# Optimization experiments

Hardware: AMD Instinct MI355X
Metric: run time of the kernel (lower is better)

Reference implementation:

```python
import jax, jax.numpy as jnp
import numpy as np
from math import sqrt

B, S, D, H = 4, 2048, 1024, 16
DH = D // H          # 64
DF = 4 * D           # 4096
EPS = 1e-5
NEG = -1e9


def layer_norm(x, w, b):
    mu = jnp.mean(x, axis=-1, keepdims=True)
    var = jnp.mean((x - mu) ** 2, axis=-1, keepdims=True)
    return (x - mu) * jax.lax.rsqrt(var + EPS) * w + b


def setup_inputs() -> dict:
    key = jax.random.key(0)
    ks = jax.random.split(key, 16)
    s = 0.02
    return {
        "state": jax.random.normal(ks[0], (B, S, D), jnp.float32),
        "mask": jax.random.randint(ks[1], (B, S), 0, 2, jnp.int32),
        "ln1_w": jnp.ones((D,), jnp.float32),
        "ln1_b": jnp.zeros((D,), jnp.float32),
        "Wq": jax.random.normal(ks[2], (H, D, DH), jnp.float32) * s,
        "bq": jnp.zeros((H, DH), jnp.float32),
        "Wk": jax.random.normal(ks[3], (H, D, DH), jnp.float32) * s,
        "bk": jnp.zeros((H, DH), jnp.float32),
        "Wv": jax.random.normal(ks[4], (H, D, DH), jnp.float32) * s,
        "bv": jnp.zeros((H, DH), jnp.float32),
        "Wo": jax.random.normal(ks[5], (D, D), jnp.float32) * s,
        "bo": jnp.zeros((D,), jnp.float32),
        "ln2_w": jnp.ones((D,), jnp.float32),
        "ln2_b": jnp.zeros((D,), jnp.float32),
        "W1": jax.random.normal(ks[6], (D, DF), jnp.float32) * s,
        "b1": jnp.zeros((DF,), jnp.float32),
        "W2": jax.random.normal(ks[7], (DF, D), jnp.float32) * s,
        "b2": jnp.zeros((D,), jnp.float32),
    }


def reference(state, mask, ln1_w, ln1_b, Wq, bq, Wk, bk, Wv, bv, Wo, bo,
              ln2_w, ln2_b, W1, b1, W2, b2):
    # pre-norm attention block
    hidden = layer_norm(state, ln1_w, ln1_b)               # [B,S,D]
    q = jnp.einsum("bsd,hde->bhse", hidden, Wq) + bq[None, :, None, :]
    k = jnp.einsum("bsd,hde->bhse", hidden, Wk) + bk[None, :, None, :]
    v = jnp.einsum("bsd,hde->bhse", hidden, Wv) + bv[None, :, None, :]
    scores = jnp.einsum("bhse,bhte->bhst", q, k) / sqrt(DH)  # [B,H,S,S]
    scores = jnp.where(mask[:, None, None, :] == 0, NEG, scores)
    weights = jax.nn.softmax(scores, axis=-1)
    attended = jnp.einsum("bhst,bhte->bhse", weights, v)    # [B,H,S,DH]
    # concat heads in head order (matches torch cat over per-head outputs)
    attended = attended.transpose(0, 2, 1, 3).reshape(B, S, D)
    attn_out = attended @ Wo + bo
    output = state + attn_out
    # pre-norm FFN block (dropout=0 -> identity)
    hidden = layer_norm(output, ln2_w, ln2_b)
    ff = jax.nn.gelu(hidden @ W1 + b1, approximate=False) @ W2 + b2
    return output + ff
```

## Files before the change

kernel.cpp:

```cpp
#include <hip/hip_runtime.h>
#include <math.h>

#define B_  4
#define S_  2048
#define D_  1024
#define H_  16
#define DH_ 64
#define DF_ 4096
#define M_  8192

#define QSC 0.18033688011112042f

typedef __attribute__((ext_vector_type(8))) short bf8_t;
typedef __attribute__((ext_vector_type(4))) float f4_t;

#if defined(__has_builtin)
#if __has_builtin(__builtin_amdgcn_cvt_pk_bf16_f32)
#define HAVE_PKCVT 1
#endif
#if __has_builtin(__builtin_amdgcn_global_load_lds)
#define HAVE_ASYNC 1
#endif
#if __has_builtin(__builtin_amdgcn_exp2f)
#define EXP2F(x) __builtin_amdgcn_exp2f(x)
#else
#define EXP2F(x) __expf((x) * 0.69314718055994531f)
#endif
#else
#define EXP2F(x) __expf((x) * 0.69314718055994531f)
#endif

__device__ __forceinline__ unsigned pk_bf16(float lo, float hi) {
#ifdef HAVE_PKCVT
  auto r = __builtin_amdgcn_cvt_pk_bf16_f32(lo, hi);
  unsigned u; __builtin_memcpy(&u, &r, 4); return u;
#else
  union { float f; unsigned u; } a, b2; a.f = lo; b2.f = hi;
  unsigned ra = a.u + 0x7fffu + ((a.u >> 16) & 1u);
  unsigned rb = b2.u + 0x7fffu + ((b2.u >> 16) & 1u);
  return (ra >> 16) | (rb & 0xffff0000u);
#endif
}

__device__ __forceinline__ unsigned short f2bf(float x) {
  return (unsigned short)(pk_bf16(x, x) & 0xffffu);
}

__device__ __forceinline__ bf8_t upk8(unsigned u0, unsigned u1, unsigned u2, unsigned u3) {
  union { unsigned u[4]; bf8_t v; } c;
  c.u[0] = u0; c.u[1] = u1; c.u[2] = u2; c.u[3] = u3; return c.v;
}

__device__ __forceinline__ f4_t mfma32(bf8_t a, bf8_t b, f4_t c) {
  return __builtin_amdgcn_mfma_f32_16x16x32_bf16(a, b, c, 0, 0, 0);
}

__device__ __forceinline__ void async16(const void* g, void* l) {
#ifdef HAVE_ASYNC
  __builtin_amdgcn_global_load_lds((__attribute__((address_space(1))) void*)(g),
                                   (__attribute__((address_space(3))) void*)(l), 16, 0, 0);
#else
  *(uint4*)l = *(const uint4*)g;
#endif
}

__device__ __forceinline__ int sw(int row) { return row & 7; }


__global__ __launch_bounds__(256) void wtrans_kernel(const float* __restrict__ in,
                                                     unsigned short* __restrict__ out,
                                                     int K, int N) {
  const int k0 = blockIdx.x * 32, n0 = blockIdx.y * 32;
  __shared__ float t[32][33];
  const int tid = threadIdx.x;
#pragma unroll
  for (int i = 0; i < 4; i++) {
    int idx = i * 256 + tid; int r = idx >> 5, c = idx & 31;
    t[r][c] = in[(size_t)(k0 + r) * N + n0 + c];
  }
  __syncthreads();
#pragma unroll
  for (int i = 0; i < 4; i++) {
    int idx = i * 256 + tid; int r = idx >> 5, c = idx & 31;
    out[(size_t)(n0 + r) * K + k0 + c] = f2bf(t[c][r]);
  }
}

__global__ __launch_bounds__(256) void qkvpack_kernel(const float* __restrict__ Wq,
                                                      const float* __restrict__ Wk,
                                                      const float* __restrict__ Wv,
                                                      unsigned short* __restrict__ WqkvT) {
  const int z = blockIdx.z;
  const int sel = z >> 4, h = z & 15;
  const float* in = (sel == 0 ? Wq : sel == 1 ? Wk : Wv) + (size_t)h * D_ * DH_;
  const int k0 = blockIdx.x * 32, n0 = blockIdx.y * 32;
  __shared__ float t[32][33];
  const int tid = threadIdx.x;
#pragma unroll
  for (int i = 0; i < 4; i++) {
    int idx = i * 256 + tid; int r = idx >> 5, c = idx & 31;
    t[r][c] = in[(size_t)(k0 + r) * DH_ + n0 + c];
  }
  __syncthreads();
#pragma unroll
  for (int i = 0; i < 4; i++) {
    int idx = i * 256 + tid; int r = idx >> 5, c = idx & 31;
    int n = sel * 1024 + h * 64 + n0 + r;
    WqkvT[(size_t)n * D_ + k0 + c] = f2bf(t[c][r]);
  }
}

__global__ void biaspack_kernel(const float* __restrict__ bq, const float* __restrict__ bk,
                                const float* __restrict__ bv, float* __restrict__ bqkv) {
  int i = blockIdx.x * 256 + threadIdx.x;
  if (i < 3072) {
    int sel = i >> 10, j = i & 1023;
    const float* src = sel == 0 ? bq : sel == 1 ? bk : bv;
    bqkv[i] = src[j];
  }
}


__global__ __launch_bounds__(256) void ln_kernel(const float* __restrict__ x,
                                                 const float* __restrict__ w,
                                                 const float* __restrict__ bb,
                                                 unsigned short* __restrict__ out) {
  const int row = blockIdx.x;
  const float* xr = x + (size_t)row * D_;
  const int tid = threadIdx.x;
  float v[4]; float s = 0.f;
#pragma unroll
  for (int i = 0; i < 4; i++) { v[i] = xr[tid + i * 256]; s += v[i]; }
  __shared__ float red[8];
#pragma unroll
  for (int o = 32; o; o >>= 1) s += __shfl_xor(s, o, 64);
  const int wv = tid >> 6, ln = tid & 63;
  if (!ln) red[wv] = s;
  __syncthreads();
  float mean = (red[0] + red[1] + red[2] + red[3]) * (1.f / 1024.f);
  float s2 = 0.f;
#pragma unroll
  for (int i = 0; i < 4; i++) { float d = v[i] - mean; s2 += d * d; }
#pragma unroll
  for (int o = 32; o; o >>= 1) s2 += __shfl_xor(s2, o, 64);
  if (!ln) red[4 + wv] = s2;
  __syncthreads();
  float var = (red[4] + red[5] + red[6] + red[7]) * (1.f / 1024.f);
  float rstd = rsqrtf(var + 1e-5f);
#pragma unroll
  for (int i = 0; i < 4; i++) {
    int c = tid + i * 256;
    out[(size_t)row * D_ + c] = f2bf((v[i] - mean) * rstd * w[c] + bb[c]);
  }
}

template <int EPI>
__global__ __launch_bounds__(256) void gemm_bt(const unsigned short* __restrict__ A,
                                               const unsigned short* __restrict__ Bt,
                                               const float* __restrict__ bias,
                                               const float* __restrict__ resid,
                                               unsigned short* __restrict__ outb,
                                               float* __restrict__ outf,
                                               unsigned short* __restrict__ vTout,
                                               int Ndim, int Kdim) {
  __shared__ __align__(16) unsigned short Asmem[4096];
  __shared__ __align__(16) unsigned short Bsmem[4096];
  const int tid = threadIdx.x;
  const int wave = tid >> 6, lane = tid & 63;
  const int quad = lane >> 4, l16 = lane & 15;
  const int wm = wave >> 1, wn = wave & 1;
  const int m0 = blockIdx.y * 128, n0 = blockIdx.x * 128;

  const f4_t fzero = {0.f, 0.f, 0.f, 0.f};
  f4_t acc[4][4];
#pragma unroll
  for (int i = 0; i < 4; i++)
#pragma unroll
    for (int j = 0; j < 4; j++) acc[i][j] = fzero;

  const int rowA = tid >> 2;
  const int kp = (tid & 3) * 8;

  for (int k0 = 0; k0 < Kdim; k0 += 32) {
    __syncthreads();
#pragma unroll
    for (int r = 0; r < 2; r++) {
      const int row = r * 64 + rowA;
      const int e = row * 32 + kp;
      async16(A  + (size_t)(m0 + row) * Kdim + k0 + kp, &Asmem[e]);
      async16(Bt + (size_t)(n0 + row) * Kdim + k0 + kp, &Bsmem[e]);
    }
    __syncthreads();

    bf8_t a[4], b[4];
#pragma unroll
    for (int i = 0; i < 4; i++) {
      a[i] = *(const bf8_t*)&Asmem[(wm * 64 + i * 16 + l16) * 32 + quad * 8];
      b[i] = *(const bf8_t*)&Bsmem[(wn * 64 + i * 16 + l16) * 32 + quad * 8];
    }
#pragma unroll
    for (int i = 0; i < 4; i++)
#pragma unroll
      for (int j = 0; j < 4; j++)
        acc[i][j] = mfma32(a[i], b[j], acc[i][j]);
  }

  const float sc = 1.f;
#pragma unroll
  for (int i = 0; i < 4; i++) {
#pragma unroll
    for (int j = 0; j < 4; j++) {
#pragma unroll
      for (int r = 0; r < 4; r++) {
        const int m = m0 + wm * 64 + i * 16 + quad * 4 + r;
        const int n = n0 + wn * 64 + j * 16 + l16;
        float v = acc[i][j][r] + bias[n];
        (void)sc;
        if constexpr (EPI == 2) v = 0.5f * v * (1.f + erff(v * 0.70710678118654752f));
        if constexpr (EPI == 1) {
          v += resid[(size_t)m * Ndim + n];
          outf[(size_t)m * Ndim + n] = v;
        } else {
          outb[(size_t)m * Ndim + n] = f2bf(v);
        }
      }
    }
  }
  (void)vTout;
}

template <int EPI>
__global__ __launch_bounds__(512, 2) void gemm256(const unsigned short* __restrict__ A,
                                                  const unsigned short* __restrict__ Bt,
                                                  const float* __restrict__ bias,
                                                  const float* __restrict__ resid,
                                                  unsigned short* __restrict__ outb,
                                                  float* __restrict__ outf,
                                                  unsigned short* __restrict__ vTout,
                                                  int Ndim, int Kdim) {
  __shared__ __align__(16) unsigned short Asm[32768];
  __shared__ __align__(16) unsigned short Bsm[32768];
  const int tid = threadIdx.x;
  const int wave = tid >> 6, lane = tid & 63;
  const int quad = lane >> 4, l16 = lane & 15;
  const int wm = wave >> 2, wn = wave & 3;

  const int gx = gridDim.x;
  const int nwg = gx * (int)gridDim.y;
  const int lin = (int)blockIdx.y * gx + (int)blockIdx.x;
  const int swz = (lin & 7) * (nwg >> 3) + (lin >> 3);
  const int m0 = (swz / gx) * 256, n0 = (swz % gx) * 256;

  const int NT = Kdim >> 6;
  const int srow = lane >> 3, schk = lane & 7;

#define STAGE_A(t, row0) do {                                                   \
    const int r_ = (row0) + srow;                                               \
    async16(A + (size_t)(m0 + r_) * Kdim + (t) * 64 + ((schk ^ (r_ & 7)) << 3), \
            &Asm[(((t) & 1) << 14) + ((row0) << 6)]); } while (0)
#define STAGE_B(t, row0) do {                                                    \
    const int r_ = (row0) + srow;                                                \
    async16(Bt + (size_t)(n0 + r_) * Kdim + (t) * 64 + ((schk ^ (r_ & 7)) << 3), \
            &Bsm[(((t) & 1) << 14) + ((row0) << 6)]); } while (0)
#define STAGE_A0(t) do { STAGE_A(t, wave * 8); STAGE_A(t, 128 + wave * 8); } while (0)
#define STAGE_A1(t) do { STAGE_A(t, 64 + wave * 8); STAGE_A(t, 192 + wave * 8); } while (0)
#define STAGE_B0(t) do { const int rb_ = (wave >> 1) * 64 + (wave & 1) * 8;  \
    STAGE_B(t, rb_); STAGE_B(t, rb_ + 16); } while (0)
#define STAGE_B1(t) do { const int rb_ = (wave >> 1) * 64 + 32 + (wave & 1) * 8; \
    STAGE_B(t, rb_); STAGE_B(t, rb_ + 16); } while (0)

#define AFR(bo, row, s) \
  (*(const bf8_t*)&Asm[(bo) + ((row) << 6) + ((((s) * 4 + quad) ^ ((row) & 7)) << 3)])
#define BFR(bo, row, s) \
  (*(const bf8_t*)&Bsm[(bo) + ((row) << 6) + ((((s) * 4 + quad) ^ ((row) & 7)) << 3)])

  const f4_t fzero = {0.f, 0.f, 0.f, 0.f};
  f4_t acc[8][4];
#pragma unroll
  for (int i = 0; i < 8; i++)
#pragma unroll
    for (int j = 0; j < 4; j++) acc[i][j] = fzero;

  STAGE_A0(0); STAGE_A1(0); STAGE_B0(0); STAGE_B1(0);
  STAGE_A0(1); STAGE_A1(1); STAGE_B0(1); STAGE_B1(1);
  asm volatile("s_waitcnt vmcnt(8)" ::: "memory");
  __builtin_amdgcn_s_barrier();

  const int ar0 = wm << 7;
  const int br0 = wn << 6;

  for (int t = 0; t < NT; ++t) {
    const int bo = (t & 1) << 14;
    const bool pf = (t + 2) < NT;
    const int t2 = t + 2;
    bf8_t af[4][2], bf0[2][2], bf1[2][2];

#pragma unroll
    for (int i = 0; i < 4; i++) {
      af[i][0] = AFR(bo, ar0 + i * 16 + l16, 0);
      af[i][1] = AFR(bo, ar0 + i * 16 + l16, 1);
    }
#pragma unroll
    for (int j = 0; j < 2; j++) {
      bf0[j][0] = BFR(bo, br0 + j * 16 + l16, 0);
      bf0[j][1] = BFR(bo, br0 + j * 16 + l16, 1);
    }
    asm volatile("s_waitcnt lgkmcnt(8)" ::: "memory");
    __builtin_amdgcn_s_barrier();
    asm volatile("s_waitcnt lgkmcnt(0)" ::: "memory");
    __builtin_amdgcn_sched_barrier(0);
    __builtin_amdgcn_s_setprio(1);
#pragma unroll
    for (int s = 0; s < 2; s++)
#pragma unroll
      for (int i = 0; i < 4; i++)
#pragma unroll
        for (int j = 0; j < 2; j++)
          acc[i][j] = mfma32(af[i][s], bf0[j][s], acc[i][j]);
    __builtin_amdgcn_s_setprio(0);
    __builtin_amdgcn_s_barrier();

#pragma unroll
    for (int j = 0; j < 2; j++) {
      bf1[j][0] = BFR(bo, br0 + 32 + j * 16 + l16, 0);
      bf1[j][1] = BFR(bo, br0 + 32 + j * 16 + l16, 1);
    }
    if (pf) { STAGE_A0(t2); STAGE_B0(t2); }
    __builtin_amdgcn_s_barrier();
    asm volatile("s_waitcnt lgkmcnt(0)" ::: "memory");
    __builtin_amdgcn_sched_barrier(0);
    __builtin_amdgcn_s_setprio(1);
#pragma unroll
    for (int s = 0; s < 2; s++)
#pragma unroll
      for (int i = 0; i < 4; i++)
#pragma unroll
        for (int j = 0; j < 2; j++)
          acc[i][2 + j] = mfma32(af[i][s], bf1[j][s], acc[i][2 + j]);
    __builtin_amdgcn_s_setprio(0);
    __builtin_amdgcn_s_barrier();

#pragma unroll
    for (int i = 0; i < 4; i++) {
      af[i][0] = AFR(bo, ar0 + 64 + i * 16 + l16, 0);
      af[i][1] = AFR(bo, ar0 + 64 + i * 16 + l16, 1);
    }
    if (pf) STAGE_B1(t2);
    __builtin_amdgcn_s_barrier();
    asm volatile("s_waitcnt lgkmcnt(0)" ::: "memory");
    __builtin_amdgcn_sched_barrier(0);
    __builtin_amdgcn_s_setprio(1);
#pragma unroll
    for (int s = 0; s < 2; s++)
#pragma unroll
      for (int i = 0; i < 4; i++)
#pragma unroll
        for (int j = 0; j < 2; j++)
          acc[4 + i][2 + j] = mfma32(af[i][s], bf1[j][s], acc[4 + i][2 + j]);
    __builtin_amdgcn_s_setprio(0);
    __builtin_amdgcn_s_barrier();

    if (pf) STAGE_A1(t2);
    __builtin_amdgcn_s_barrier();
    __builtin_amdgcn_s_setprio(1);
#pragma unroll
    for (int s = 0; s < 2; s++)
#pragma unroll
      for (int i = 0; i < 4; i++)
#pragma unroll
        for (int j = 0; j < 2; j++)
          acc[4 + i][j] = mfma32(af[i][s], bf0[j][s], acc[4 + i][j]);
    __builtin_amdgcn_s_setprio(0);
    if (pf) asm volatile("s_waitcnt vmcnt(8)" ::: "memory");
    else    asm volatile("s_waitcnt vmcnt(0)" ::: "memory");
    __builtin_amdgcn_s_barrier();
  }

#undef STAGE_A
#undef STAGE_B
#undef STAGE_A0
#undef STAGE_A1
#undef STAGE_B0
#undef STAGE_B1
#undef AFR
#undef BFR

  if (EPI == 0 && n0 >= 2048) {
    const int bb2 = m0 >> 11;
    const int sb64 = (m0 & 2047) + (wm << 7);
#pragma unroll
    for (int mi = 0; mi < 8; mi++) {
      const int i4 = mi & 3;
      const int g0 = (i4 & 2) * 16 + 8 * quad + 4 * (i4 & 1);
      const int sbase = sb64 + (mi >> 2) * 64 + g0;
#pragma unroll
      for (int nj = 0; nj < 4; nj++) {
        const int n = n0 + wn * 64 + nj * 16 + l16;
        const int ef = n - 2048;
        const int hh = ef >> 6, e = ef & 63;
        const float bsv = bias[n];
        uint2 wq;
        wq.x = pk_bf16(acc[mi][nj][0] + bsv, acc[mi][nj][1] + bsv);
        wq.y = pk_bf16(acc[mi][nj][2] + bsv, acc[mi][nj][3] + bsv);
        *(uint2*)&vTout[(size_t)((bb2 * 16 + hh) * 64 + e) * S_ + sbase] = wq;
      }
    }
    return;
  }

  const float sc = (EPI == 0 && n0 < 1024) ? QSC : 1.f;
#pragma unroll
  for (int mi = 0; mi < 8; mi++) {
#pragma unroll
    for (int nj = 0; nj < 4; nj++) {
#pragma unroll
      for (int r = 0; r < 4; r++) {
        const int m = m0 + wm * 128 + mi * 16 + quad * 4 + r;
        const int n = n0 + wn * 64 + nj * 16 + l16;
        float v = acc[mi][nj][r] + bias[n];
        if constexpr (EPI == 0) v *= sc;
        if constexpr (EPI == 2) v = 0.5f * v * (1.f + erff(v * 0.70710678118654752f));
        if constexpr (EPI == 1) {
          v += resid[(size_t)m * Ndim + n];
          outf[(size_t)m * Ndim + n] = v;
        } else {
          outb[(size_t)m * Ndim + n] = f2bf(v);
        }
      }
    }
  }
}


__global__ __launch_bounds__(256) void attn_kernel(const unsigned short* __restrict__ qkv,
                                                   const unsigned short* __restrict__ vT,
                                                   const int* __restrict__ maskp,
                                                   unsigned short* __restrict__ attended) {
  const int bh = blockIdx.y, b = bh >> 4, h = bh & 15;
  const int q0 = blockIdx.x * 128;
  const int tid = threadIdx.x, wv = tid >> 6, lane = tid & 63;
  const int quad = lane >> 4, l16 = lane & 15;
  __shared__ __align__(16) unsigned short smem[16384];
  __shared__ float biasl[128];
  unsigned short* Ks = smem;
  unsigned short* Vs = smem + 8192;

  bf8_t aq[2][2];
#pragma unroll
  for (int sb = 0; sb < 2; sb++) {
    const unsigned short* qrow =
        qkv + (size_t)(b * S_ + q0 + wv * 32 + sb * 16 + l16) * 3072 + h * 64;
    aq[sb][0] = *(const bf8_t*)(qrow + quad * 8);
    aq[sb][1] = *(const bf8_t*)(qrow + 32 + quad * 8);
  }

  const bf8_t ones8 = {0x3F80, 0x3F80, 0x3F80, 0x3F80, 0x3F80, 0x3F80, 0x3F80, 0x3F80};
  const f4_t fzero = {0.f, 0.f, 0.f, 0.f};
  f4_t o[2][4], lacc[2];
#pragma unroll
  for (int sb = 0; sb < 2; sb++) {
    lacc[sb] = fzero;
#pragma unroll
    for (int ee = 0; ee < 4; ee++) o[sb][ee] = fzero;
  }

  for (int t0 = 0; t0 < S_; t0 += 128) {
    __syncthreads();
#pragma unroll
    for (int r = 0; r < 4; r++) {
      int ci = r * 256 + tid;
      int krow = ci >> 3, kc = (ci & 7) ^ sw(krow);
      async16(qkv + (size_t)(b * S_ + t0 + krow) * 3072 + 1024 + h * 64 + kc * 8,
              &Ks[ci * 8]);
      int e = ci >> 4, half = (ci >> 3) & 1, vc = (ci & 7) ^ sw(e);
      async16(vT + (size_t)(bh * 64 + e) * S_ + t0 + half * 64 + vc * 8,
              &Vs[ci * 8]);
    }
    if (tid < 128) biasl[tid] = maskp[b * S_ + t0 + tid] ? 0.f : -8e9f;
    __syncthreads();

#pragma unroll
    for (int th = 0; th < 2; th++) {
      f4_t sf[2][4];
#pragma unroll
      for (int jj = 0; jj < 4; jj++) {
        f4_t bi = *(const f4_t*)&biasl[th * 64 + jj * 16 + quad * 4];
        sf[0][jj] = bi;
        sf[1][jj] = bi;
      }
#pragma unroll
      for (int jj = 0; jj < 4; jj++) {
        int krow = th * 64 + jj * 16 + l16, sk = sw(krow);
        bf8_t kf0 = *(const bf8_t*)&Ks[krow * 64 + (quad ^ sk) * 8];
        bf8_t kf1 = *(const bf8_t*)&Ks[krow * 64 + ((quad + 4) ^ sk) * 8];
        sf[0][jj] = mfma32(kf0, aq[0][0], sf[0][jj]);
        sf[0][jj] = mfma32(kf1, aq[0][1], sf[0][jj]);
        sf[1][jj] = mfma32(kf0, aq[1][0], sf[1][jj]);
        sf[1][jj] = mfma32(kf1, aq[1][1], sf[1][jj]);
      }

      bf8_t pp[2][2];
#pragma unroll
      for (int sb = 0; sb < 2; sb++) {
#pragma unroll
        for (int h2 = 0; h2 < 2; h2++) {
          float p0 = EXP2F(sf[sb][2 * h2][0]),     p1 = EXP2F(sf[sb][2 * h2][1]);
          float p2 = EXP2F(sf[sb][2 * h2][2]),     p3 = EXP2F(sf[sb][2 * h2][3]);
          float p4 = EXP2F(sf[sb][2 * h2 + 1][0]), p5 = EXP2F(sf[sb][2 * h2 + 1][1]);
          float p6 = EXP2F(sf[sb][2 * h2 + 1][2]), p7 = EXP2F(sf[sb][2 * h2 + 1][3]);
          pp[sb][h2] = upk8(pk_bf16(p0, p1), pk_bf16(p2, p3),
                            pk_bf16(p4, p5), pk_bf16(p6, p7));
        }
        lacc[sb] = mfma32(ones8, pp[sb][0], lacc[sb]);
        lacc[sb] = mfma32(ones8, pp[sb][1], lacc[sb]);
      }

#pragma unroll
      for (int ee = 0; ee < 4; ee++) {
        int vrow = ee * 16 + l16, sv = sw(vrow);
#pragma unroll
        for (int h2 = 0; h2 < 2; h2++) {
          bf8_t vf = *(const bf8_t*)&Vs[vrow * 128 + th * 64 + ((4 * h2 + quad) ^ sv) * 8];
          o[0][ee] = mfma32(vf, pp[0][h2], o[0][ee]);
          o[1][ee] = mfma32(vf, pp[1][h2], o[1][ee]);
        }
      }
    }
  }

  float linv[2];
#pragma unroll
  for (int sb = 0; sb < 2; sb++) linv[sb] = 1.f / lacc[sb][0];

  __syncthreads();
  unsigned short* Os = smem;
#pragma unroll
  for (int sb = 0; sb < 2; sb++) {
    int srow = wv * 32 + sb * 16 + l16;
#pragma unroll
    for (int ee = 0; ee < 4; ee++) {
      unsigned w0 = pk_bf16(o[sb][ee][0] * linv[sb], o[sb][ee][1] * linv[sb]);
      unsigned w1 = pk_bf16(o[sb][ee][2] * linv[sb], o[sb][ee][3] * linv[sb]);
      uint2 wq; wq.x = w0; wq.y = w1;
      *(uint2*)&Os[srow * 72 + ee * 16 + quad * 4] = wq;
    }
  }
  __syncthreads();
#pragma unroll
  for (int it = 0; it < 4; it++) {
    int row = it * 32 + (tid >> 3), e0 = (tid & 7) * 8;
    bf8_t v = *(const bf8_t*)&Os[row * 72 + e0];
    *(bf8_t*)&attended[(size_t)(b * S_ + q0 + row) * D_ + h * 64 + e0] = v;
  }
}


extern "C" void kernel_launch(void* const* d_in, const int* in_sizes, int n_in,
                              void* d_out, int out_size, void* d_ws, size_t ws_size,
                              hipStream_t stream) {
  const float* state = (const float*)d_in[0];
  const int*   maskp = (const int*)d_in[1];
  const float* ln1w  = (const float*)d_in[2];
  const float* ln1b  = (const float*)d_in[3];
  const float* Wq    = (const float*)d_in[4];
  const float* bq    = (const float*)d_in[5];
  const float* Wk    = (const float*)d_in[6];
  const float* bk    = (const float*)d_in[7];
  const float* Wv    = (const float*)d_in[8];
  const float* bv    = (const float*)d_in[9];
  const float* Wo    = (const float*)d_in[10];
  const float* bo    = (const float*)d_in[11];
  const float* ln2w  = (const float*)d_in[12];
  const float* ln2b  = (const float*)d_in[13];
  const float* W1    = (const float*)d_in[14];
  const float* b1    = (const float*)d_in[15];
  const float* W2    = (const float*)d_in[16];
  const float* b2    = (const float*)d_in[17];

  char* w = (char*)d_ws;
  unsigned short* hidden = (unsigned short*)w; w += (size_t)M_ * D_ * 2;
  unsigned short* qkv    = (unsigned short*)w; w += (size_t)M_ * 3072 * 2;
  unsigned short* vT     = (unsigned short*)w; w += (size_t)M_ * D_ * 2;
  float*          outp   = (float*)w;          w += (size_t)M_ * D_ * 4;
  unsigned short* WqkvT  = (unsigned short*)w; w += (size_t)3072 * D_ * 2;
  unsigned short* WoT    = (unsigned short*)w; w += (size_t)D_ * D_ * 2;
  unsigned short* W1T    = (unsigned short*)w; w += (size_t)DF_ * D_ * 2;
  unsigned short* W2T    = (unsigned short*)w; w += (size_t)D_ * DF_ * 2;
  float*          bqkv   = (float*)w;          w += 3072 * 4;
  unsigned short* ff1    = qkv;

  qkvpack_kernel<<<dim3(32, 2, 48), 256, 0, stream>>>(Wq, Wk, Wv, WqkvT);
  wtrans_kernel<<<dim3(32, 32), 256, 0, stream>>>(Wo, WoT, D_, D_);
  wtrans_kernel<<<dim3(32, 128), 256, 0, stream>>>(W1, W1T, D_, DF_);
  wtrans_kernel<<<dim3(128, 32), 256, 0, stream>>>(W2, W2T, DF_, D_);
  biaspack_kernel<<<12, 256, 0, stream>>>(bq, bk, bv, bqkv);

  ln_kernel<<<M_, 256, 0, stream>>>(state, ln1w, ln1b, hidden);
  gemm256<0><<<dim3(3072 / 256, M_ / 256), 512, 0, stream>>>(hidden, WqkvT, bqkv, nullptr,
                                                             qkv, nullptr, vT, 3072, D_);
  attn_kernel<<<dim3(S_ / 128, B_ * H_), 256, 0, stream>>>(qkv, vT, maskp, hidden);
  gemm_bt<1><<<dim3(D_ / 128, M_ / 128), 256, 0, stream>>>(hidden, WoT, bo, state,
                                                           nullptr, outp, nullptr, D_, D_);
  ln_kernel<<<M_, 256, 0, stream>>>(outp, ln2w, ln2b, hidden);
  gemm256<2><<<dim3(DF_ / 256, M_ / 256), 512, 0, stream>>>(hidden, W1T, b1, nullptr,
                                                            ff1, nullptr, nullptr, DF_, D_);
  gemm_bt<1><<<dim3(D_ / 128, M_ / 128), 256, 0, stream>>>(ff1, W2T, b2, outp,
                                                           nullptr, (float*)d_out, nullptr, D_, DF_);
}
```

Measured before the change: 597.4 us.

## Split-K the FFN down-projection on the 256-tile GEMM and add reduction kernel

The second FFN GEMM (K=4096, N=1024) now runs on the larger 256x256 tile kernel with split-K of 2 along a new grid z dimension. Each half writes fp32 partials into separate buffers, and a small elementwise kernel adds the partials, residual and bias. The aim is to keep enough workgroups in flight for an N=1024 output while using the more efficient tile kernel. It also adds grouped block swizzling to the 128-tile GEMM used by the output projection. In exchange it pays extra fp32 traffic for the partials and one more kernel launch, and it reorders workspace buffers so the partial buffer can reuse the hidden region.

```diff
diff --git a/kernel.cpp b/kernel.cpp
--- a/kernel.cpp
+++ b/kernel.cpp
@@ -154,6 +154,18 @@
   }
 }
 
+__global__ __launch_bounds__(256) void ffn2red_kernel(float* __restrict__ out,
+                                                      const float* __restrict__ P,
+                                                      const float* __restrict__ resid,
+                                                      const float* __restrict__ bias) {
+  const size_t i = ((size_t)blockIdx.x * 256 + threadIdx.x) * 4;
+  f4_t a  = *(const f4_t*)&out[i];
+  f4_t p  = *(const f4_t*)&P[i];
+  f4_t rr = *(const f4_t*)&resid[i];
+  f4_t bb = *(const f4_t*)&bias[(int)(i & 1023)];
+  *(f4_t*)&out[i] = a + p + rr + bb;
+}
+
 template <int EPI>
 __global__ __launch_bounds__(256) void gemm_bt(const unsigned short* __restrict__ A,
                                                const unsigned short* __restrict__ Bt,
@@ -161,7 +173,6 @@
                                                const float* __restrict__ resid,
                                                unsigned short* __restrict__ outb,
                                                float* __restrict__ outf,
-                                               unsigned short* __restrict__ vTout,
                                                int Ndim, int Kdim) {
   __shared__ __align__(16) unsigned short Asmem[4096];
   __shared__ __align__(16) unsigned short Bsmem[4096];
@@ -169,7 +180,12 @@
   const int wave = tid >> 6, lane = tid & 63;
   const int quad = lane >> 4, l16 = lane & 15;
   const int wm = wave >> 1, wn = wave & 1;
-  const int m0 = blockIdx.y * 128, n0 = blockIdx.x * 128;
+
+  const int gx = gridDim.x;
+  const int nwg = gx * (int)gridDim.y;
+  const int lin = (int)blockIdx.y * gx + (int)blockIdx.x;
+  const int swz = (lin & 7) * (nwg >> 3) + (lin >> 3);
+  const int m0 = (swz / gx) * 128, n0 = (swz % gx) * 128;
 
   const f4_t fzero = {0.f, 0.f, 0.f, 0.f};
   f4_t acc[4][4];
@@ -205,7 +221,6 @@
         acc[i][j] = mfma32(a[i], b[j], acc[i][j]);
   }
 
-  const float sc = 1.f;
 #pragma unroll
   for (int i = 0; i < 4; i++) {
 #pragma unroll
@@ -215,7 +230,6 @@
         const int m = m0 + wm * 64 + i * 16 + quad * 4 + r;
         const int n = n0 + wn * 64 + j * 16 + l16;
         float v = acc[i][j][r] + bias[n];
-        (void)sc;
         if constexpr (EPI == 2) v = 0.5f * v * (1.f + erff(v * 0.70710678118654752f));
         if constexpr (EPI == 1) {
           v += resid[(size_t)m * Ndim + n];
@@ -226,7 +240,6 @@
       }
     }
   }
-  (void)vTout;
 }
 
 template <int EPI>
@@ -236,8 +249,9 @@
                                                   const float* __restrict__ resid,
                                                   unsigned short* __restrict__ outb,
                                                   float* __restrict__ outf,
+                                                  float* __restrict__ outf2,
                                                   unsigned short* __restrict__ vTout,
-                                                  int Ndim, int Kdim) {
+                                                  int Ndim, int Kdim, int Kstride) {
   __shared__ __align__(16) unsigned short Asm[32768];
   __shared__ __align__(16) unsigned short Bsm[32768];
   const int tid = threadIdx.x;
@@ -250,17 +264,20 @@
   const int lin = (int)blockIdx.y * gx + (int)blockIdx.x;
   const int swz = (lin & 7) * (nwg >> 3) + (lin >> 3);
   const int m0 = (swz / gx) * 256, n0 = (swz % gx) * 256;
+  const int kz = (int)blockIdx.z * Kdim;
 
   const int NT = Kdim >> 6;
   const int srow = lane >> 3, schk = lane & 7;
 
-#define STAGE_A(t, row0) do {                                                   \
-    const int r_ = (row0) + srow;                                               \
-    async16(A + (size_t)(m0 + r_) * Kdim + (t) * 64 + ((schk ^ (r_ & 7)) << 3), \
+#define STAGE_A(t, row0) do {                                               \
+    const int r_ = (row0) + srow;                                           \
+    async16(A + (size_t)(m0 + r_) * Kstride + kz + (t) * 64 +               \
+                ((schk ^ (r_ & 7)) << 3),                                   \
             &Asm[(((t) & 1) << 14) + ((row0) << 6)]); } while (0)
-#define STAGE_B(t, row0) do {                                                    \
-    const int r_ = (row0) + srow;                                                \
-    async16(Bt + (size_t)(n0 + r_) * Kdim + (t) * 64 + ((schk ^ (r_ & 7)) << 3), \
+#define STAGE_B(t, row0) do {                                               \
+    const int r_ = (row0) + srow;                                           \
+    async16(Bt + (size_t)(n0 + r_) * Kstride + kz + (t) * 64 +              \
+                 ((schk ^ (r_ & 7)) << 3),                                  \
             &Bsm[(((t) & 1) << 14) + ((row0) << 6)]); } while (0)
 #define STAGE_A0(t) do { STAGE_A(t, wave * 8); STAGE_A(t, 128 + wave * 8); } while (0)
 #define STAGE_A1(t) do { STAGE_A(t, 64 + wave * 8); STAGE_A(t, 192 + wave * 8); } while (0)
@@ -408,21 +425,25 @@
     return;
   }
 
+  float* const pdst = (EPI == 3) ? (blockIdx.z ? outf2 : outf) : outf;
   const float sc = (EPI == 0 && n0 < 1024) ? QSC : 1.f;
 #pragma unroll
   for (int mi = 0; mi < 8; mi++) {
 #pragma unroll
     for (int nj = 0; nj < 4; nj++) {
+      const int n = n0 + wn * 64 + nj * 16 + l16;
+      const float bs = (EPI == 3) ? 0.f : bias[n];
 #pragma unroll
       for (int r = 0; r < 4; r++) {
         const int m = m0 + wm * 128 + mi * 16 + quad * 4 + r;
-        const int n = n0 + wn * 64 + nj * 16 + l16;
-        float v = acc[mi][nj][r] + bias[n];
+        float v = acc[mi][nj][r] + bs;
         if constexpr (EPI == 0) v *= sc;
         if constexpr (EPI == 2) v = 0.5f * v * (1.f + erff(v * 0.70710678118654752f));
         if constexpr (EPI == 1) {
           v += resid[(size_t)m * Ndim + n];
           outf[(size_t)m * Ndim + n] = v;
+        } else if constexpr (EPI == 3) {
+          pdst[(size_t)m * Ndim + n] = v;
         } else {
           outb[(size_t)m * Ndim + n] = f2bf(v);
         }
@@ -579,15 +600,16 @@
 
   char* w = (char*)d_ws;
   unsigned short* hidden = (unsigned short*)w; w += (size_t)M_ * D_ * 2;
+  unsigned short* WqkvT  = (unsigned short*)w; w += (size_t)3072 * D_ * 2;
+  unsigned short* WoT    = (unsigned short*)w; w += (size_t)D_ * D_ * 2;
+  unsigned short* W1T    = (unsigned short*)w; w += (size_t)DF_ * D_ * 2;
   unsigned short* qkv    = (unsigned short*)w; w += (size_t)M_ * 3072 * 2;
   unsigned short* vT     = (unsigned short*)w; w += (size_t)M_ * D_ * 2;
   float*          outp   = (float*)w;          w += (size_t)M_ * D_ * 4;
-  unsigned short* WqkvT  = (unsigned short*)w; w += (size_t)3072 * D_ * 2;
-  unsigned short* WoT    = (unsigned short*)w; w += (size_t)D_ * D_ * 2;
-  unsigned short* W1T    = (unsigned short*)w; w += (size_t)DF_ * D_ * 2;
   unsigned short* W2T    = (unsigned short*)w; w += (size_t)D_ * DF_ * 2;
   float*          bqkv   = (float*)w;          w += 3072 * 4;
   unsigned short* ff1    = qkv;
+  float*          Pbuf   = (float*)hidden;
 
   qkvpack_kernel<<<dim3(32, 2, 48), 256, 0, stream>>>(Wq, Wk, Wv, WqkvT);
   wtrans_kernel<<<dim3(32, 32), 256, 0, stream>>>(Wo, WoT, D_, D_);
@@ -596,14 +618,16 @@
   biaspack_kernel<<<12, 256, 0, stream>>>(bq, bk, bv, bqkv);
 
   ln_kernel<<<M_, 256, 0, stream>>>(state, ln1w, ln1b, hidden);
-  gemm256<0><<<dim3(3072 / 256, M_ / 256), 512, 0, stream>>>(hidden, WqkvT, bqkv, nullptr,
-                                                             qkv, nullptr, vT, 3072, D_);
+  gemm256<0><<<dim3(3072 / 256, M_ / 256), 512, 0, stream>>>(
+      hidden, WqkvT, bqkv, nullptr, qkv, nullptr, nullptr, vT, 3072, D_, D_);
   attn_kernel<<<dim3(S_ / 128, B_ * H_), 256, 0, stream>>>(qkv, vT, maskp, hidden);
   gemm_bt<1><<<dim3(D_ / 128, M_ / 128), 256, 0, stream>>>(hidden, WoT, bo, state,
-                                                           nullptr, outp, nullptr, D_, D_);
+                                                           nullptr, outp, D_, D_);
   ln_kernel<<<M_, 256, 0, stream>>>(outp, ln2w, ln2b, hidden);
-  gemm256<2><<<dim3(DF_ / 256, M_ / 256), 512, 0, stream>>>(hidden, W1T, b1, nullptr,
-                                                            ff1, nullptr, nullptr, DF_, D_);
-  gemm_bt<1><<<dim3(D_ / 128, M_ / 128), 256, 0, stream>>>(ff1, W2T, b2, outp,
-                                                           nullptr, (float*)d_out, nullptr, D_, DF_);
-}
+  gemm256<2><<<dim3(DF_ / 256, M_ / 256), 512, 0, stream>>>(
+      hidden, W1T, b1, nullptr, ff1, nullptr, nullptr, nullptr, DF_, D_, D_);
+  gemm256<3><<<dim3(D_ / 256, M_ / 256, 2), 512, 0, stream>>>(
+      ff1, W2T, nullptr, nullptr, nullptr, Pbuf, (float*)d_out, nullptr,
+      D_, DF_ / 2, DF_);
+  ffn2red_kernel<<<(M_ * D_) / 1024, 256, 0, stream>>>((float*)d_out, Pbuf, outp, b2);
+}
```

Measured after the change: 570.4 us. 4.5% less time.
